# Kernel optimization log

Measured on AMD Instinct MI355X. Metric: run time of the kernel, lower is better.

The kernel has to match this reference:

```python
import jax, jax.numpy as jnp
import numpy as np

N, D, E, R, G, M = 8192, 1024, 64, 64, 8, 8

def setup_inputs() -> dict:
    key = jax.random.key(0)
    k_h, k_wg, k_wl, k_w1, k_w2 = jax.random.split(key, 5)
    return {
        'h': jax.random.normal(k_h, (N, D), jnp.float32),
        'Wg': jax.random.normal(k_wg, (D, G), jnp.float32) * 0.02,  # nn.Linear weight (transposed)
        'bg': jnp.zeros((G,), jnp.float32),
        'Wloc': jax.random.normal(k_wl, (G, D, M), jnp.float32) * 0.02,
        'W1': jax.random.normal(k_w1, (E, D, R), jnp.float32) * 0.02,
        'W2': jax.random.normal(k_w2, (E, R, D), jnp.float32) * 0.02,
        'k': 2,
    }

def reference(h, Wg, bg, Wloc, W1, W2, k):
    n, d = h.shape
    g, _, m = Wloc.shape
    e = W1.shape[0]
    router_temp = 1.0
    # stage 1: group routing (top-1)
    g_scores = h @ Wg + bg                                   # (N, G)
    group_idx = jnp.argmax(g_scores, axis=-1)                # (N,)
    # stage 2: within-group scores; compute all groups (cheap: N*G*M) then select
    all_local = jnp.einsum('nd,gdm->ngm', h, Wloc)           # (N, G, M)
    local_scores = jnp.take_along_axis(all_local, group_idx[:, None, None], axis=1)[:, 0]  # (N, M)
    topv, topm = jax.lax.top_k(local_scores, k)              # (N, k)
    gate = jax.nn.softmax(topv / max(router_temp, 1e-6), axis=-1)
    expert_ids = group_idx[:, None] * m + topm               # (N, k) global expert ids
    # scatter gates into dense (N, E); topm entries are distinct per token
    gate_full = jnp.zeros((n, e), h.dtype).at[jnp.arange(n)[:, None], expert_ids].set(gate)
    # low-rank expert compute: relu(h @ W1) @ W2, weighted-combined
    tmp = jax.nn.relu(jnp.einsum('nd,edr->ner', h, W1))      # (N, E, R)
    out = jnp.einsum('ner,erd->nd', gate_full[:, :, None] * tmp, W2)  # (N, D)
    return out, expert_ids, gate, group_idx
```

## Files before the change

### kernel.cpp

```cpp
#include <hip/hip_runtime.h>
#include <hip/hip_bf16.h>
#include <cstdint>
#include <cstddef>

#define NTOK 8192
#define DIM  1024
#define NEXP 64
#define RANK 64
#define NGRP 8
#define NLOC 8
#define ECAP 2048

typedef __attribute__((ext_vector_type(8))) short bf16x8;
typedef __attribute__((ext_vector_type(4))) float f32x4;

static __device__ inline unsigned int pack_bf16x2(float a, float b) {
    __hip_bfloat16 ha = __float2bfloat16(a);
    __hip_bfloat16 hb = __float2bfloat16(b);
    return (unsigned int)(*(unsigned short*)&ha) |
           ((unsigned int)(*(unsigned short*)&hb) << 16);
}

__global__ __launch_bounds__(512) void score_all(
    const float* __restrict__ h, const float* __restrict__ Wg,
    const float* __restrict__ Wloc, unsigned short* __restrict__ hb,
    float* __restrict__ Sp)
{
    __shared__ float Hs[64][66];
    __shared__ float Ws[40][72];

    const int tile = blockIdx.x;
    const int slab = blockIdx.y;
    const int z    = blockIdx.z;
    const int tid  = threadIdx.x;
    const int wave = tid >> 6;
    const int lane = tid & 63;
    const int t0   = tile * 64;
    const int kz   = z * 512;

    const int r0  = tid >> 3;
    const int seg = (tid & 7) * 8;

    float acc[5] = {};

    float4 hpre[2];
    float4 wgp;
    float4 wlp;

    {
        const int kb = kz;
        const float* src = h + (size_t)(t0 + r0) * DIM + kb + seg;
        hpre[0] = *(const float4*)(src);
        hpre[1] = *(const float4*)(src + 4);
        const int g = tid >> 7, r = tid & 127;
        if (slab == 0) {
            if (tid < 128)
                wgp = *(const float4*)(Wg + (size_t)(kb + (tid >> 1)) * NGRP + (tid & 1) * 4);
            wlp = *(const float4*)(Wloc + (size_t)g * (DIM * NLOC)
                                       + (size_t)(kb + (r >> 1)) * NLOC + (r & 1) * 4);
        } else {
            wlp = *(const float4*)(Wloc + (size_t)(4 + g) * (DIM * NLOC)
                                       + (size_t)(kb + (r >> 1)) * NLOC + (r & 1) * 4);
        }
    }

    for (int chunk = 0; chunk < 8; ++chunk) {
        const int kb = kz + chunk * 64;

        {
            float* dst = &Hs[r0][seg];
#pragma unroll
            for (int q = 0; q < 2; ++q) {
                const float4 v = hpre[q];
                *(float2*)(dst + q * 4)     = make_float2(v.x, v.y);
                *(float2*)(dst + q * 4 + 2) = make_float2(v.z, v.w);
            }
            if (slab == 0) {
                unsigned short* hrow = hb + (size_t)(t0 + r0) * DIM + kb + seg;
#pragma unroll
                for (int q = 0; q < 2; ++q) {
                    const float4 v = hpre[q];
                    uint2 pk;
                    pk.x = pack_bf16x2(v.x, v.y);
                    pk.y = pack_bf16x2(v.z, v.w);
                    *(uint2*)(hrow + q * 4) = pk;
                }
            }
        }
        {
            const int g = tid >> 7, r = tid & 127;
            const int k = r >> 1;
            if (slab == 0) {
                if (tid < 128) {
                    const int kk = tid >> 1, m4 = (tid & 1) * 4;
                    Ws[m4 + 0][kk] = wgp.x; Ws[m4 + 1][kk] = wgp.y;
                    Ws[m4 + 2][kk] = wgp.z; Ws[m4 + 3][kk] = wgp.w;
                }
                const int c = 8 + g * 8 + (r & 1) * 4;
                Ws[c + 0][k] = wlp.x; Ws[c + 1][k] = wlp.y;
                Ws[c + 2][k] = wlp.z; Ws[c + 3][k] = wlp.w;
            } else {
                const int c = g * 8 + (r & 1) * 4;
                Ws[c + 0][k] = wlp.x; Ws[c + 1][k] = wlp.y;
                Ws[c + 2][k] = wlp.z; Ws[c + 3][k] = wlp.w;
            }
        }
        __syncthreads();

        if (chunk < 7) {
            const int kbn = kb + 64;
            const float* src = h + (size_t)(t0 + r0) * DIM + kbn + seg;
            hpre[0] = *(const float4*)(src);
            hpre[1] = *(const float4*)(src + 4);
            const int g = tid >> 7, r = tid & 127;
            if (slab == 0) {
                if (tid < 128)
                    wgp = *(const float4*)(Wg + (size_t)(kbn + (tid >> 1)) * NGRP + (tid & 1) * 4);
                wlp = *(const float4*)(Wloc + (size_t)g * (DIM * NLOC)
                                           + (size_t)(kbn + (r >> 1)) * NLOC + (r & 1) * 4);
            } else {
                wlp = *(const float4*)(Wloc + (size_t)(4 + g) * (DIM * NLOC)
                                           + (size_t)(kbn + (r >> 1)) * NLOC + (r & 1) * 4);
            }
        }

        if (slab == 0) {
            const int c0 = wave * 5;
#pragma unroll 4
            for (int kq = 0; kq < 16; ++kq) {
                const int k0 = kq * 4;
                const float2 a00 = *(const float2*)&Hs[lane][k0];
                const float2 a01 = *(const float2*)&Hs[lane][k0 + 2];
                float4 bq[5];
#pragma unroll
                for (int c = 0; c < 5; ++c)
                    bq[c] = *(const float4*)&Ws[c0 + c][k0];
#pragma unroll
                for (int c = 0; c < 5; ++c) acc[c] += a00.x * bq[c].x;
#pragma unroll
                for (int c = 0; c < 5; ++c) acc[c] += a00.y * bq[c].y;
#pragma unroll
                for (int c = 0; c < 5; ++c) acc[c] += a01.x * bq[c].z;
#pragma unroll
                for (int c = 0; c < 5; ++c) acc[c] += a01.y * bq[c].w;
            }
        } else {
            const int c0 = wave * 4;
#pragma unroll 4
            for (int kq = 0; kq < 16; ++kq) {
                const int k0 = kq * 4;
                const float2 a00 = *(const float2*)&Hs[lane][k0];
                const float2 a01 = *(const float2*)&Hs[lane][k0 + 2];
                float4 bq[4];
#pragma unroll
                for (int c = 0; c < 4; ++c)
                    bq[c] = *(const float4*)&Ws[c0 + c][k0];
#pragma unroll
                for (int c = 0; c < 4; ++c) acc[c] += a00.x * bq[c].x;
#pragma unroll
                for (int c = 0; c < 4; ++c) acc[c] += a00.y * bq[c].y;
#pragma unroll
                for (int c = 0; c < 4; ++c) acc[c] += a01.x * bq[c].z;
#pragma unroll
                for (int c = 0; c < 4; ++c) acc[c] += a01.y * bq[c].w;
            }
        }
        __syncthreads();
    }

    const int gcol = (slab ? 40 + wave * 4 : wave * 5);
    const int nout = slab ? 4 : 5;
    float* dstS = Sp + (size_t)z * (NTOK * 72) + (size_t)(t0 + lane) * 72 + gcol;
#pragma unroll
    for (int c = 0; c < 5; ++c)
        if (c < nout) dstS[c] = acc[c];
}

__global__ __launch_bounds__(256) void route_all(
    const float* __restrict__ Sp, const float* __restrict__ bg,
    float* __restrict__ out_gidx, float* __restrict__ out_eid,
    float* __restrict__ out_gate, int* __restrict__ cursor,
    int* __restrict__ token_list, float* __restrict__ slot_gate)
{
    const int t = blockIdx.x * 256 + threadIdx.x;
    const float* p0 = Sp + (size_t)t * 72;
    const float* p1 = p0 + (size_t)NTOK * 72;
    float s[72];
#pragma unroll
    for (int i = 0; i < 18; ++i) {
        const float4 a = *(const float4*)(p0 + i * 4);
        const float4 b = *(const float4*)(p1 + i * 4);
        s[i * 4 + 0] = a.x + b.x; s[i * 4 + 1] = a.y + b.y;
        s[i * 4 + 2] = a.z + b.z; s[i * 4 + 3] = a.w + b.w;
    }

    int gi = 0; float best = s[0] + bg[0];
#pragma unroll
    for (int g = 1; g < NGRP; ++g) {
        const float v = s[g] + bg[g];
        if (v > best) { best = v; gi = g; }
    }

    float ls[NLOC];
#pragma unroll
    for (int m = 0; m < NLOC; ++m) ls[m] = s[8 + gi * NLOC + m];

    int m1 = 0; float v1 = ls[0];
#pragma unroll
    for (int m = 1; m < NLOC; ++m) { if (ls[m] > v1) { v1 = ls[m]; m1 = m; } }
    int m2 = (m1 == 0) ? 1 : 0; float v2 = ls[m2];
#pragma unroll
    for (int m = 0; m < NLOC; ++m) {
        if (m != m1 && m != ((m1 == 0) ? 1 : 0) && ls[m] > v2) { v2 = ls[m]; m2 = m; }
    }
    const float e2v = expf(v2 - v1);
    const float inv = 1.f / (1.f + e2v);
    const float g0 = inv, g1 = e2v * inv;
    const int ea = gi * NLOC + m1, eb = gi * NLOC + m2;

    out_gidx[t] = (float)gi;
    out_eid[t * 2 + 0] = (float)ea;
    out_eid[t * 2 + 1] = (float)eb;
    out_gate[t * 2 + 0] = g0;
    out_gate[t * 2 + 1] = g1;

    const int pA = atomicAdd(&cursor[ea], 1);
    if (pA < ECAP) {
        token_list[ea * ECAP + pA] = t * 2 + 0;
        slot_gate[ea * ECAP + pA] = g0;
    }
    const int pB = atomicAdd(&cursor[eb], 1);
    if (pB < ECAP) {
        token_list[eb * ECAP + pB] = t * 2 + 1;
        slot_gate[eb * ECAP + pB] = g1;
    }
}

__global__ __launch_bounds__(256) void prep_w(
    const float* __restrict__ W1, const float* __restrict__ W2,
    unsigned short* __restrict__ W1t, unsigned short* __restrict__ W2t)
{
    __shared__ float Ls[64][65];
    const int e = blockIdx.x;
    const int y = blockIdx.y;
    if (y < 16) {
        const int kb = y;
        const float* src = W1 + (size_t)e * DIM * RANK + (size_t)kb * 64 * RANK;
#pragma unroll
        for (int it = 0; it < 4; ++it) {
            const int kk = (threadIdx.x >> 4) + it * 16;
            const int rr = (threadIdx.x & 15) * 4;
            *(float4*)&Ls[kk][rr] = *(const float4*)(src + (size_t)kk * RANK + rr);
        }
        __syncthreads();
#pragma unroll
        for (int it = 0; it < 2; ++it) {
            const int idx = threadIdx.x + it * 256;
            const int r = idx >> 3, k8 = (idx & 7) * 8;
            uint4 v;
            v.x = pack_bf16x2(Ls[k8 + 0][r], Ls[k8 + 1][r]);
            v.y = pack_bf16x2(Ls[k8 + 2][r], Ls[k8 + 3][r]);
            v.z = pack_bf16x2(Ls[k8 + 4][r], Ls[k8 + 5][r]);
            v.w = pack_bf16x2(Ls[k8 + 6][r], Ls[k8 + 7][r]);
            *(uint4*)(W1t + (size_t)e * RANK * DIM + (size_t)r * DIM + kb * 64 + k8) = v;
        }
    } else {
        const int db = y - 16;
        const float* src = W2 + (size_t)e * RANK * DIM + db * 64;
#pragma unroll
        for (int it = 0; it < 4; ++it) {
            const int rr = (threadIdx.x >> 4) + it * 16;
            const int dd = (threadIdx.x & 15) * 4;
            *(float4*)&Ls[rr][dd] = *(const float4*)(src + (size_t)rr * DIM + dd);
        }
        __syncthreads();
#pragma unroll
        for (int it = 0; it < 2; ++it) {
            const int idx = threadIdx.x + it * 256;
            const int d = idx >> 3, r8 = (idx & 7) * 8;
            uint4 v;
            v.x = pack_bf16x2(Ls[r8 + 0][d], Ls[r8 + 1][d]);
            v.y = pack_bf16x2(Ls[r8 + 2][d], Ls[r8 + 3][d]);
            v.z = pack_bf16x2(Ls[r8 + 4][d], Ls[r8 + 5][d]);
            v.w = pack_bf16x2(Ls[r8 + 6][d], Ls[r8 + 7][d]);
            *(uint4*)(W2t + (size_t)e * DIM * RANK + (size_t)(db * 64 + d) * RANK + r8) = v;
        }
    }
}

__global__ __launch_bounds__(256, 2) void e12_mfma(
    const unsigned short* __restrict__ hb, const unsigned short* __restrict__ W1t,
    const unsigned short* __restrict__ W2t, const int* __restrict__ counts,
    const int* __restrict__ token_list, const float* __restrict__ slot_gate,
    float* __restrict__ out, float* __restrict__ contrib)
{
    __shared__ unsigned short Hs[64 * 72];
    __shared__ unsigned short Ws[64 * 72];
    __shared__ unsigned short Ps[64 * 72];
    __shared__ unsigned short W2s[64 * 72];
    __shared__ int   tokS[64];
    __shared__ float gateS[64];

    const int e    = blockIdx.x;
    const int tid  = threadIdx.x;
    const int ne   = min(counts[e], ECAP);
    const int base = e * ECAP;

    const unsigned short* W1te = W1t + (size_t)e * RANK * DIM;
    const unsigned short* W2te = W2t + (size_t)e * DIM * RANK;
    const int wave = tid >> 6;
    const int lane = tid & 63;
    const int tx   = lane & 15;
    const int quad = lane >> 4;

    for (int tile = blockIdx.y; tile * 64 < ne; tile += 8) {
        const int row0 = tile * 64;
        __syncthreads();
        if (tid < 64) {
            const int gr = row0 + tid;
            tokS[tid]  = (gr < ne) ? token_list[base + gr] : -1;
            gateS[tid] = (gr < ne) ? slot_gate[base + gr] : 0.f;
        }

        f32x4 acc[4] = {};
        for (int kc = 0; kc < DIM; kc += 64) {
            __syncthreads();
#pragma unroll
            for (int it = 0; it < 2; ++it) {
                const int idx = tid + it * 256;
                const int s = idx >> 3, k8 = (idx & 7) * 8;
                const int ent = tokS[s];
                uint4 v = make_uint4(0, 0, 0, 0);
                if (ent >= 0)
                    v = *(const uint4*)(hb + (size_t)(ent >> 1) * DIM + kc + k8);
                *(uint4*)(Hs + s * 72 + k8) = v;
            }
#pragma unroll
            for (int it = 0; it < 2; ++it) {
                const int idx = tid + it * 256;
                const int r = idx >> 3, k8 = (idx & 7) * 8;
                *(uint4*)(Ws + r * 72 + k8) =
                    *(const uint4*)(W1te + (size_t)r * DIM + kc + k8);
            }
            __syncthreads();
#pragma unroll
            for (int ks = 0; ks < 2; ++ks) {
                const bf16x8 a = *(const bf16x8*)(Hs + (wave * 16 + tx) * 72 + ks * 32 + quad * 8);
#pragma unroll
                for (int j = 0; j < 4; ++j) {
                    const bf16x8 b = *(const bf16x8*)(Ws + (j * 16 + tx) * 72 + ks * 32 + quad * 8);
                    acc[j] = __builtin_amdgcn_mfma_f32_16x16x32_bf16(a, b, acc[j], 0, 0, 0);
                }
            }
        }

#pragma unroll
        for (int j = 0; j < 4; ++j) {
#pragma unroll
            for (int i = 0; i < 4; ++i) {
                const int sl = wave * 16 + quad * 4 + i;
                const float v = fmaxf(acc[j][i], 0.f) * gateS[sl];
                __hip_bfloat16 hv = __float2bfloat16(v);
                Ps[sl * 72 + j * 16 + tx] = *(unsigned short*)&hv;
            }
        }
        __syncthreads();

        for (int cb = 0; cb < 16; ++cb) {
            const int colbase = cb * 64;
#pragma unroll
            for (int it = 0; it < 2; ++it) {
                const int idx = tid + it * 256;
                const int d = idx >> 3, r8 = (idx & 7) * 8;
                *(uint4*)(W2s + d * 72 + r8) =
                    *(const uint4*)(W2te + (size_t)(colbase + d) * RANK + r8);
            }
            __syncthreads();
            f32x4 acc2[4] = {};
#pragma unroll
            for (int ks = 0; ks < 2; ++ks) {
                const bf16x8 a = *(const bf16x8*)(Ps + (wave * 16 + tx) * 72 + ks * 32 + quad * 8);
#pragma unroll
                for (int j = 0; j < 4; ++j) {
                    const bf16x8 b = *(const bf16x8*)(W2s + (j * 16 + tx) * 72 + ks * 32 + quad * 8);
                    acc2[j] = __builtin_amdgcn_mfma_f32_16x16x32_bf16(a, b, acc2[j], 0, 0, 0);
                }
            }
#pragma unroll
            for (int i = 0; i < 4; ++i) {
                const int sl = wave * 16 + quad * 4 + i;
                const int ent = tokS[sl];
                if (ent >= 0) {
                    float* basep = (ent & 1) ? contrib : out;
                    float* op = basep + (size_t)(ent >> 1) * DIM + colbase;
#pragma unroll
                    for (int j = 0; j < 4; ++j)
                        op[j * 16 + tx] = acc2[j][i];
                }
            }
            __syncthreads();
        }
    }
}

__global__ __launch_bounds__(256) void combine_kernel(
    const float* __restrict__ contrib, float* __restrict__ out)
{
    const size_t i = (size_t)blockIdx.x * 256 + threadIdx.x;
    float4 a = ((const float4*)out)[i];
    const float4 b = ((const float4*)contrib)[i];
    a.x += b.x; a.y += b.y; a.z += b.z; a.w += b.w;
    ((float4*)out)[i] = a;
}

extern "C" void kernel_launch(void* const* d_in, const int* in_sizes, int n_in,
                              void* d_out, int out_size, void* d_ws, size_t ws_size,
                              hipStream_t stream)
{
    const float* h    = (const float*)d_in[0];
    const float* Wg   = (const float*)d_in[1];
    const float* bg   = (const float*)d_in[2];
    const float* Wloc = (const float*)d_in[3];
    const float* W1   = (const float*)d_in[4];
    const float* W2   = (const float*)d_in[5];

    float* out_f    = (float*)d_out;
    float* out_main = out_f;
    float* out_eid  = out_f + (size_t)NTOK * DIM;
    float* out_gate = out_eid + (size_t)NTOK * 2;
    float* out_gidx = out_gate + (size_t)NTOK * 2;

    int* ws_i        = (int*)d_ws;
    int* cursor_e    = ws_i;
    int* token_list  = ws_i + 1024;
    float* slot_gate = (float*)(ws_i + 1024 + NEXP * ECAP);
    float* Sp        = slot_gate + NEXP * ECAP;
    unsigned short* hb  = (unsigned short*)(Sp + (size_t)2 * NTOK * 72);
    unsigned short* W1t = hb + (size_t)NTOK * DIM;
    unsigned short* W2t = W1t + (size_t)NEXP * RANK * DIM;
    float* contrib      = (float*)(W2t + (size_t)NEXP * DIM * RANK);

    hipMemsetAsync(cursor_e, 0, 64 * sizeof(int), stream);

    prep_w<<<dim3(NEXP, 32), 256, 0, stream>>>(W1, W2, W1t, W2t);
    score_all<<<dim3(128, 2, 2), 512, 0, stream>>>(h, Wg, Wloc, hb, Sp);
    route_all<<<NTOK / 256, 256, 0, stream>>>(Sp, bg, out_gidx, out_eid,
        out_gate, cursor_e, token_list, slot_gate);
    e12_mfma<<<dim3(NEXP, 8), 256, 0, stream>>>(hb, W1t, W2t, cursor_e,
        token_list, slot_gate, out_main, contrib);
    combine_kernel<<<(NTOK * DIM / 4) / 256, 256, 0, stream>>>(contrib, out_main);
}
```

Measured before the change: 235.9 us.

## Load MFMA operands directly from global memory and halve expert-kernel tile blocks

The expert GEMM kernel stops staging H, W1 and W2 tiles through shared memory. Each lane now reads its bf16x8 MFMA fragments straight from global memory, which removes most block-wide barriers; the intermediate P tile still goes through LDS, but each wave only reads rows it wrote itself. The grid's y-dimension drops from 8 to 4 tile-strided blocks per expert. The intent is to cut LDS traffic and barrier stalls. In exchange, the four waves each reload the same weight rows through cache with strided 16-byte accesses, and fewer blocks are launched, which lowers parallelism.

Result: slower. 281.1 us (+19.1%).

```diff
diff --git a/kernel.cpp b/kernel.cpp
--- a/kernel.cpp
+++ b/kernel.cpp
@@ -294,10 +294,7 @@
     const int* __restrict__ token_list, const float* __restrict__ slot_gate,
     float* __restrict__ out, float* __restrict__ contrib)
 {
-    __shared__ unsigned short Hs[64 * 72];
-    __shared__ unsigned short Ws[64 * 72];
     __shared__ unsigned short Ps[64 * 72];
-    __shared__ unsigned short W2s[64 * 72];
     __shared__ int   tokS[64];
     __shared__ float gateS[64];
 
@@ -313,7 +310,7 @@
     const int tx   = lane & 15;
     const int quad = lane >> 4;
 
-    for (int tile = blockIdx.y; tile * 64 < ne; tile += 8) {
+    for (int tile = blockIdx.y; tile * 64 < ne; tile += 4) {
         const int row0 = tile * 64;
         __syncthreads();
         if (tid < 64) {
@@ -321,34 +318,24 @@
             tokS[tid]  = (gr < ne) ? token_list[base + gr] : -1;
             gateS[tid] = (gr < ne) ? slot_gate[base + gr] : 0.f;
         }
+        __syncthreads();
+
+        const int entA = tokS[wave * 16 + tx];
+        const unsigned short* arow =
+            (entA >= 0) ? (hb + (size_t)(entA >> 1) * DIM) : nullptr;
 
         f32x4 acc[4] = {};
+        const bf16x8 zero8 = {};
+#pragma unroll 2
         for (int kc = 0; kc < DIM; kc += 64) {
-            __syncthreads();
-#pragma unroll
-            for (int it = 0; it < 2; ++it) {
-                const int idx = tid + it * 256;
-                const int s = idx >> 3, k8 = (idx & 7) * 8;
-                const int ent = tokS[s];
-                uint4 v = make_uint4(0, 0, 0, 0);
-                if (ent >= 0)
-                    v = *(const uint4*)(hb + (size_t)(ent >> 1) * DIM + kc + k8);
-                *(uint4*)(Hs + s * 72 + k8) = v;
-            }
-#pragma unroll
-            for (int it = 0; it < 2; ++it) {
-                const int idx = tid + it * 256;
-                const int r = idx >> 3, k8 = (idx & 7) * 8;
-                *(uint4*)(Ws + r * 72 + k8) =
-                    *(const uint4*)(W1te + (size_t)r * DIM + kc + k8);
-            }
-            __syncthreads();
 #pragma unroll
             for (int ks = 0; ks < 2; ++ks) {
-                const bf16x8 a = *(const bf16x8*)(Hs + (wave * 16 + tx) * 72 + ks * 32 + quad * 8);
+                const int ko = kc + ks * 32 + quad * 8;
+                const bf16x8 a = arow ? *(const bf16x8*)(arow + ko) : zero8;
 #pragma unroll
                 for (int j = 0; j < 4; ++j) {
-                    const bf16x8 b = *(const bf16x8*)(Ws + (j * 16 + tx) * 72 + ks * 32 + quad * 8);
+                    const bf16x8 b =
+                        *(const bf16x8*)(W1te + (size_t)(j * 16 + tx) * DIM + ko);
                     acc[j] = __builtin_amdgcn_mfma_f32_16x16x32_bf16(a, b, acc[j], 0, 0, 0);
                 }
             }
@@ -364,25 +351,20 @@
                 Ps[sl * 72 + j * 16 + tx] = *(unsigned short*)&hv;
             }
         }
-        __syncthreads();
-
+
+        const int entO = tokS[wave * 16 + quad * 4 + 0];
+        (void)entO;
         for (int cb = 0; cb < 16; ++cb) {
             const int colbase = cb * 64;
-#pragma unroll
-            for (int it = 0; it < 2; ++it) {
-                const int idx = tid + it * 256;
-                const int d = idx >> 3, r8 = (idx & 7) * 8;
-                *(uint4*)(W2s + d * 72 + r8) =
-                    *(const uint4*)(W2te + (size_t)(colbase + d) * RANK + r8);
-            }
-            __syncthreads();
             f32x4 acc2[4] = {};
 #pragma unroll
             for (int ks = 0; ks < 2; ++ks) {
                 const bf16x8 a = *(const bf16x8*)(Ps + (wave * 16 + tx) * 72 + ks * 32 + quad * 8);
 #pragma unroll
                 for (int j = 0; j < 4; ++j) {
-                    const bf16x8 b = *(const bf16x8*)(W2s + (j * 16 + tx) * 72 + ks * 32 + quad * 8);
+                    const bf16x8 b =
+                        *(const bf16x8*)(W2te + (size_t)(colbase + j * 16 + tx) * RANK
+                                              + ks * 32 + quad * 8);
                     acc2[j] = __builtin_amdgcn_mfma_f32_16x16x32_bf16(a, b, acc2[j], 0, 0, 0);
                 }
             }
@@ -398,7 +380,6 @@
                         op[j * 16 + tx] = acc2[j][i];
                 }
             }
-            __syncthreads();
         }
     }
 }
@@ -446,7 +427,7 @@
     score_all<<<dim3(128, 2, 2), 512, 0, stream>>>(h, Wg, Wloc, hb, Sp);
     route_all<<<NTOK / 256, 256, 0, stream>>>(Sp, bg, out_gidx, out_eid,
         out_gate, cursor_e, token_list, slot_gate);
-    e12_mfma<<<dim3(NEXP, 8), 256, 0, stream>>>(hb, W1t, W2t, cursor_e,
+    e12_mfma<<<dim3(NEXP, 4), 256, 0, stream>>>(hb, W1t, W2t, cursor_e,
         token_list, slot_gate, out_main, contrib);
     combine_kernel<<<(NTOK * DIM / 4) / 256, 256, 0, stream>>>(contrib, out_main);
 }
```
